# Kernel optimization log

Hardware: AMD Instinct MI355X
Metric: run time of the kernel (lower is better)

The kernel has to match this reference:

```python
import jax, jax.numpy as jnp
import numpy as np

B, S, H, E = 8, 512, 1024, 8
T = B * S            # total tokens
CAP = T // E         # capacity, capacity_factor = 1.0


def _moe(x, wg, ew1, eb1, ew2, eb2):
    # x: [T, H] tokens; top-1 gating with capacity, DeepSpeed-style dispatch/combine
    gates = jax.nn.softmax(x @ wg)                      # [T, E]
    idx = jnp.argmax(gates, axis=-1)                    # [T]
    mask1 = jax.nn.one_hot(idx, E, dtype=x.dtype)       # [T, E]
    locations = jnp.cumsum(mask1, axis=0) - 1.0         # position within expert queue
    mask1 = mask1 * (locations < CAP).astype(x.dtype)   # drop overflow tokens
    gates1 = jnp.sum(gates * mask1, axis=-1)            # [T] combine weight
    locs = jnp.sum(locations * mask1, axis=-1).astype(jnp.int32)  # [T]
    loc_oh = jax.nn.one_hot(locs, CAP, dtype=x.dtype)   # [T, C]
    combine = gates1[:, None, None] * mask1[:, :, None] * loc_oh[:, None, :]  # [T,E,C]
    dispatch = (combine > 0).astype(x.dtype)            # [T, E, C]
    xd = jnp.einsum('sec,sm->ecm', dispatch, x)         # gather tokens per expert
    h = jnp.einsum('ecm,emn->ecn', xd, ew1) + eb1[:, None, :]
    h = jnp.einsum('ecn,enp->ecp', h, ew2) + eb2[:, None, :]
    return jnp.einsum('sec,ecm->sm', combine, h)        # scatter back, weighted


def setup_inputs() -> dict:
    key = jax.random.key(0)
    ks = jax.random.split(key, 16)
    w = lambda k, shape: jax.random.normal(k, shape, jnp.float32) * 0.02
    return {
        'x': jax.random.normal(ks[0], (B, S, H), jnp.float32),
        'y': jax.random.randint(ks[1], (B,), 0, H),
        'w1': w(ks[2], (H, H)), 'b1': jnp.zeros((H,), jnp.float32),
        'w2': w(ks[3], (H, H)), 'b2': jnp.zeros((H,), jnp.float32),
        'w3': w(ks[4], (H, H)), 'b3': jnp.zeros((H,), jnp.float32),
        'wg1': w(ks[5], (H, E)),
        'e1_w1': w(ks[6], (E, H, H)), 'e1_b1': jnp.zeros((E, H), jnp.float32),
        'e1_w2': w(ks[7], (E, H, H)), 'e1_b2': jnp.zeros((E, H), jnp.float32),
        'wg2': w(ks[8], (H, E)),
        'e2_w1': w(ks[9], (E, H, H)), 'e2_b1': jnp.zeros((E, H), jnp.float32),
        'e2_w2': w(ks[10], (E, H, H)), 'e2_b2': jnp.zeros((E, H), jnp.float32),
    }


def reference(x, y, w1, b1, w2, b2, w3, b3, wg1, e1_w1, e1_b1, e1_w2, e1_b2,
              wg2, e2_w1, e2_b1, e2_w2, e2_b2):
    xf = x.reshape(-1, H)                               # [T, H]
    hidden = xf @ w1 + b1
    out = _moe(hidden, wg1, e1_w1, e1_b1, e1_w2, e1_b2)
    out = out @ w2 + b2
    out = _moe(out, wg2, e2_w1, e2_b1, e2_w2, e2_b2)
    out = out @ w3 + b3
    hidden = hidden + out
    sent = hidden.reshape(B, S, H).mean(axis=1)         # [B, H] logits
    logp = jax.nn.log_softmax(sent, axis=-1)
    return -jnp.mean(logp[jnp.arange(B), y])
```

## Files before the change

kernel.cpp:

```cpp
#include <hip/hip_runtime.h>

#define TOK 4096
#define HID 1024
#define NEXP 8
#define CAP 512
#define WSZ 1048576

typedef _Float16 f16;
typedef f16 f16x8 __attribute__((ext_vector_type(8)));
typedef f16 f16x4 __attribute__((ext_vector_type(4)));
typedef f16 f16x2 __attribute__((ext_vector_type(2)));
typedef float f32x4 __attribute__((ext_vector_type(4)));

typedef const __attribute__((address_space(1))) void gvoid;
typedef __attribute__((address_space(3))) void lvoid;

__device__ __forceinline__ void gld16(const void* g, void* l) {
  __builtin_amdgcn_global_load_lds((gvoid*)g, (lvoid*)l, 16, 0, 0);
}

template<int MODE>
__global__ __launch_bounds__(512, 1) void gemm_fused(
    const f16* __restrict__ A, const f16* __restrict__ Bt,
    const float* __restrict__ bias, f16* __restrict__ C,
    const int* __restrict__ rowmap, const float* __restrict__ gmax,
    int rowsPerExpert, long bStride, int biasStride,
    const float* __restrict__ tsrc, f16* __restrict__ tdst, int nGemm)
{
  __shared__ __align__(16) unsigned char smem[65536];
  const int tid = threadIdx.x;

  if ((int)blockIdx.x >= nGemm) {
    float (*t)[65] = (float (*)[65])smem;
    const int tb = blockIdx.x - nGemm;
    const int mat = tb >> 7, t7 = tb & 127;
    const int nb = (t7 & 7) * 128, kb = (t7 >> 3) * 64;
    const float* src = tsrc + (size_t)mat * WSZ;
    f16* d = tdst + (size_t)mat * WSZ;
    const int half = tid >> 8, tl = tid & 255;
    const int rr = tl >> 4, c4 = (tl & 15) * 4;
    float (*th)[65] = t + half * 64;
    float4 v[4];
    #pragma unroll
    for (int p = 0; p < 4; ++p)
      v[p] = *(const float4*)&src[(size_t)(kb + p * 16 + rr) * HID + nb + half * 64 + c4];
    #pragma unroll
    for (int p = 0; p < 4; ++p) {
      th[p * 16 + rr][c4 + 0] = v[p].x;
      th[p * 16 + rr][c4 + 1] = v[p].y;
      th[p * 16 + rr][c4 + 2] = v[p].z;
      th[p * 16 + rr][c4 + 3] = v[p].w;
    }
    __syncthreads();
    #pragma unroll
    for (int it = 0; it < 2; ++it) {
      const int p = it * 256 + tl;
      const int n = p >> 3, kc = p & 7;
      f16x8 o;
      #pragma unroll
      for (int j = 0; j < 8; ++j) o[j] = (f16)th[kc * 8 + j][n];
      *(f16x8*)&d[(size_t)(nb + half * 64 + n) * HID + kb + kc * 8] = o;
    }
    return;
  }

  f16* As0 = (f16*)smem;
  f16* Bs0 = (f16*)(smem + 32768);
  const int w = tid >> 6, l = tid & 63;
  const int wr = w >> 2, wc = w & 3;

  const int orig = blockIdx.x;
  const int sw = (orig & 7) * 32 + (orig >> 3);
  const int bx = sw & 7, by = sw >> 3;
  const int e = (by * 128) / rowsPerExpert;

  const int lr = l >> 3;
  const int chunkSw = ((l & 7) ^ lr) * 8;

  const f16* pst[4];
  if (w < 4) {
    #pragma unroll
    for (int i = 0; i < 4; ++i) {
      int r = by * 128 + w * 32 + i * 8 + lr;
      long tok = r;
      if (MODE == 1) { int t = rowmap[r]; tok = (t < 0) ? (long)TOK : (long)t; }
      pst[i] = A + tok * HID + chunkSw;
    }
  } else {
    #pragma unroll
    for (int i = 0; i < 4; ++i)
      pst[i] = Bt + (size_t)e * bStride
             + (size_t)(bx * 128 + (w - 4) * 32 + i * 8 + lr) * HID + chunkSw;
  }

  f32x4 acc[4][2];
  #pragma unroll
  for (int i = 0; i < 4; ++i)
    #pragma unroll
    for (int j = 0; j < 2; ++j) acc[i][j] = (f32x4){0.f, 0.f, 0.f, 0.f};

  const int g = l >> 4, c = l & 15, sa = c & 7;

  {
    f16* db = (w < 4) ? As0 + (w * 32) * 64 : Bs0 + ((w - 4) * 32) * 64;
    #pragma unroll
    for (int i = 0; i < 4; ++i) gld16(pst[i], db + i * 8 * 64);
  }

  int cur = 0;
  for (int t = 0; t < 15; ++t) {
    {
      const int k0 = (t + 1) * 64;
      f16* db = (w < 4) ? As0 + ((cur ^ 1) * 8192) + (w * 32) * 64
                        : Bs0 + ((cur ^ 1) * 8192) + ((w - 4) * 32) * 64;
      #pragma unroll
      for (int i = 0; i < 4; ++i) gld16(pst[i] + k0, db + i * 8 * 64);
    }
    asm volatile("s_waitcnt vmcnt(4)" ::: "memory");
    asm volatile("s_barrier" ::: "memory");
    __builtin_amdgcn_s_setprio(1);
    #pragma unroll
    for (int h = 0; h < 2; ++h) {
      const int q = ((h * 4 + g) ^ sa) * 8;
      f16x8 af[4], bf[2];
      #pragma unroll
      for (int mi = 0; mi < 4; ++mi)
        af[mi] = *(const f16x8*)&As0[cur * 8192 + (wr * 64 + mi * 16 + c) * 64 + q];
      #pragma unroll
      for (int ni = 0; ni < 2; ++ni)
        bf[ni] = *(const f16x8*)&Bs0[cur * 8192 + (wc * 32 + ni * 16 + c) * 64 + q];
      #pragma unroll
      for (int mi = 0; mi < 4; ++mi)
        #pragma unroll
        for (int ni = 0; ni < 2; ++ni)
          acc[mi][ni] = __builtin_amdgcn_mfma_f32_16x16x32_f16(
              af[mi], bf[ni], acc[mi][ni], 0, 0, 0);
    }
    __builtin_amdgcn_s_setprio(0);
    asm volatile("s_barrier" ::: "memory");
    cur ^= 1;
  }
  asm volatile("s_waitcnt vmcnt(0)" ::: "memory");
  asm volatile("s_barrier" ::: "memory");
  __builtin_amdgcn_s_setprio(1);
  #pragma unroll
  for (int h = 0; h < 2; ++h) {
    const int q = ((h * 4 + g) ^ sa) * 8;
    f16x8 af[4], bf[2];
    #pragma unroll
    for (int mi = 0; mi < 4; ++mi)
      af[mi] = *(const f16x8*)&As0[cur * 8192 + (wr * 64 + mi * 16 + c) * 64 + q];
    #pragma unroll
    for (int ni = 0; ni < 2; ++ni)
      bf[ni] = *(const f16x8*)&Bs0[cur * 8192 + (wc * 32 + ni * 16 + c) * 64 + q];
    #pragma unroll
    for (int mi = 0; mi < 4; ++mi)
      #pragma unroll
      for (int ni = 0; ni < 2; ++ni)
        acc[mi][ni] = __builtin_amdgcn_mfma_f32_16x16x32_f16(
            af[mi], bf[ni], acc[mi][ni], 0, 0, 0);
  }
  __builtin_amdgcn_s_setprio(0);

  int tk[4][4];
  float gv[4][4];
  if (MODE == 2) {
    #pragma unroll
    for (int mi = 0; mi < 4; ++mi)
      #pragma unroll
      for (int rr = 0; rr < 4; ++rr) {
        int r = by * 128 + wr * 64 + mi * 16 + g * 4 + rr;
        int t = rowmap[r];
        tk[mi][rr] = t;
        gv[mi][rr] = (t >= 0) ? gmax[t] : 0.f;
      }
  }
  #pragma unroll
  for (int ni = 0; ni < 2; ++ni) {
    const int col = bx * 128 + wc * 32 + ni * 16 + c;
    const float bv = bias[(size_t)e * biasStride + col];
    #pragma unroll
    for (int mi = 0; mi < 4; ++mi) {
      #pragma unroll
      for (int rr = 0; rr < 4; ++rr) {
        const float v = acc[mi][ni][rr] + bv;
        if (MODE == 2) {
          if (tk[mi][rr] >= 0)
            C[(size_t)tk[mi][rr] * HID + col] = (f16)(v * gv[mi][rr]);
        } else {
          const int row = by * 128 + wr * 64 + mi * 16 + g * 4 + rr;
          C[(size_t)row * HID + col] = (f16)v;
        }
      }
    }
  }
}

__global__ __launch_bounds__(256) void prep2(
    const float* __restrict__ x, f16* __restrict__ X0,
    f16* __restrict__ c1, f16* __restrict__ c2,
    f16* __restrict__ p1, f16* __restrict__ p2,
    const float* __restrict__ w1, const float* __restrict__ w2,
    const float* __restrict__ w3, f16* __restrict__ WT)
{
  __shared__ float t[64][65];
  const int tid = threadIdx.x;
  if ((int)blockIdx.x < 2048) {
    const f16x8 zz = {0, 0, 0, 0, 0, 0, 0, 0};
    #pragma unroll
    for (int it = 0; it < 2; ++it) {
      const size_t i = (size_t)blockIdx.x * 256 + tid + (size_t)it * 524288;
      float4 v = *(const float4*)&x[i * 4];
      f16x4 o = {(f16)v.x, (f16)v.y, (f16)v.z, (f16)v.w};
      *(f16x4*)&X0[i * 4] = o;
      if (i < 524288) { ((f16x8*)c1)[i] = zz; ((f16x8*)c2)[i] = zz; }
      if (i < 128)    { ((f16x8*)p1)[i] = zz; ((f16x8*)p2)[i] = zz; }
    }
    return;
  }
  const int zb = blockIdx.x - 2048;
  const int z = zb >> 8, t7 = zb & 255;
  const float* src = (z == 0) ? w1 : (z == 1) ? w2 : w3;
  f16* d = WT + (size_t)z * WSZ;
  const int kb = (t7 >> 4) * 64, nb = (t7 & 15) * 64;
  const int rr = tid >> 4, c4 = (tid & 15) * 4;
  float4 v[4];
  #pragma unroll
  for (int p = 0; p < 4; ++p)
    v[p] = *(const float4*)&src[(size_t)(kb + p * 16 + rr) * HID + nb + c4];
  #pragma unroll
  for (int p = 0; p < 4; ++p) {
    t[p * 16 + rr][c4 + 0] = v[p].x;
    t[p * 16 + rr][c4 + 1] = v[p].y;
    t[p * 16 + rr][c4 + 2] = v[p].z;
    t[p * 16 + rr][c4 + 3] = v[p].w;
  }
  __syncthreads();
  #pragma unroll
  for (int half = 0; half < 2; ++half) {
    const int p = half * 256 + tid;
    const int n = p >> 3, kc = p & 7;
    f16x8 o;
    #pragma unroll
    for (int j = 0; j < 8; ++j) o[j] = (f16)t[kc * 8 + j][n];
    *(f16x8*)&d[(size_t)(nb + n) * HID + kb + kc * 8] = o;
  }
}

__global__ __launch_bounds__(256) void gate_kernel(
    const f16* __restrict__ act, const float* __restrict__ wg,
    int* __restrict__ idx, float* __restrict__ gmax)
{
  const int tid = threadIdx.x;
  const int tok = blockIdx.x * 8 + (tid >> 5);
  const int sl = tid & 31;
  const f16* row = act + (size_t)tok * HID + sl * 32;
  float xv[32];
  #pragma unroll
  for (int v = 0; v < 4; ++v) {
    f16x8 hv = *(const f16x8*)(row + v * 8);
    #pragma unroll
    for (int j = 0; j < 8; ++j) xv[v * 8 + j] = (float)hv[j];
  }
  float p[NEXP];
  #pragma unroll
  for (int e = 0; e < NEXP; ++e) p[e] = 0.f;
  const float4* w4 = (const float4*)(wg + (size_t)(sl * 32) * NEXP);
  #pragma unroll
  for (int j = 0; j < 32; ++j) {
    float4 lo = w4[2 * j], hi = w4[2 * j + 1];
    p[0] += xv[j] * lo.x; p[1] += xv[j] * lo.y;
    p[2] += xv[j] * lo.z; p[3] += xv[j] * lo.w;
    p[4] += xv[j] * hi.x; p[5] += xv[j] * hi.y;
    p[6] += xv[j] * hi.z; p[7] += xv[j] * hi.w;
  }
  #pragma unroll
  for (int m = 1; m < 32; m <<= 1) {
    #pragma unroll
    for (int e = 0; e < NEXP; ++e) p[e] += __shfl_xor(p[e], m, 64);
  }
  if (sl == 0) {
    float mx = p[0]; int am = 0;
    #pragma unroll
    for (int e = 1; e < NEXP; ++e)
      if (p[e] > mx) { mx = p[e]; am = e; }
    float s = 0.f;
    #pragma unroll
    for (int e = 0; e < NEXP; ++e) s += expf(p[e] - mx);
    idx[tok] = am;
    gmax[tok] = 1.f / s;
  }
}

__global__ __launch_bounds__(512) void scan_kernel(
    const int* __restrict__ idx, int* __restrict__ rowmap)
{
  __shared__ int sidx[TOK];
  const int tid = threadIdx.x;
  for (int i = tid; i < TOK; i += 512) sidx[i] = idx[i];
  for (int i = tid; i < NEXP * CAP; i += 512) rowmap[i] = -1;
  __syncthreads();
  const int wave = tid >> 6, lane = tid & 63;
  int running = 0;
  for (int ch = 0; ch < TOK / 64; ++ch) {
    int t = ch * 64 + lane;
    bool flag = (sidx[t] == wave);
    unsigned long long m = __ballot(flag);
    int pos = running + __popcll(m & ((1ull << lane) - 1ull));
    if (flag && pos < CAP) rowmap[wave * CAP + pos] = t;
    running += __popcll(m);
  }
}

__global__ __launch_bounds__(256) void meanHC_kernel(
    const f16* __restrict__ Hb, const f16* __restrict__ C2b,
    float* __restrict__ pH, float* __restrict__ pC)
{
  const int h2 = blockIdx.x * 256 + threadIdx.x;
  const int b = blockIdx.y, sc = blockIdx.z;
  const f16x2* pa = (const f16x2*)(Hb + ((size_t)b * 512 + sc * 32) * HID) + h2;
  const f16x2* pc = (const f16x2*)(C2b + ((size_t)b * 512 + sc * 32) * HID) + h2;
  float a0 = 0.f, a1 = 0.f, c0 = 0.f, c1 = 0.f;
  #pragma unroll 4
  for (int s = 0; s < 32; ++s) {
    f16x2 va = pa[(size_t)s * 512];
    f16x2 vc = pc[(size_t)s * 512];
    a0 += (float)va[0]; a1 += (float)va[1];
    c0 += (float)vc[0]; c1 += (float)vc[1];
  }
  float* oh = pH + ((size_t)sc * 8 + b) * HID;
  float* oc = pC + ((size_t)sc * 8 + b) * HID;
  oh[h2 * 2] = a0; oh[h2 * 2 + 1] = a1;
  oc[h2 * 2] = c0; oc[h2 * 2 + 1] = c1;
}

__global__ __launch_bounds__(256) void sent_kernel(
    const float* __restrict__ pH, const float* __restrict__ pC,
    const f16* __restrict__ WT2, const float* __restrict__ b3,
    float* __restrict__ sent)
{
  __shared__ float c2m[HID];
  const int tid = threadIdx.x;
  const int b = blockIdx.x >> 2, ch = blockIdx.x & 3;
  for (int kk = tid; kk < HID; kk += 256) {
    float s = 0.f;
    #pragma unroll
    for (int sc = 0; sc < 16; ++sc) s += pC[((size_t)sc * 8 + b) * HID + kk];
    c2m[kk] = s * (1.f / 512.f);
  }
  __syncthreads();
  const int col = ch * 256 + tid;
  float hv = 0.f;
  #pragma unroll
  for (int sc = 0; sc < 16; ++sc) hv += pH[((size_t)sc * 8 + b) * HID + col];
  float acc = hv * (1.f / 512.f) + b3[col];
  const f16* wrow = WT2 + (size_t)col * HID;
  for (int k0 = 0; k0 < HID; k0 += 8) {
    f16x8 wv = *(const f16x8*)(wrow + k0);
    #pragma unroll
    for (int j = 0; j < 8; ++j) acc += c2m[k0 + j] * (float)wv[j];
  }
  sent[b * HID + col] = acc;
}

__global__ __launch_bounds__(1024) void loss_kernel(
    const float* __restrict__ sent, const int* __restrict__ y,
    float* __restrict__ out)
{
  __shared__ float red[17];
  const int tid = threadIdx.x;
  const int wid = tid >> 6, lane = tid & 63;
  float loss = 0.0f;
  for (int b = 0; b < 8; ++b) {
    const float v = sent[b * HID + tid];
    float m = v;
    #pragma unroll
    for (int o = 32; o; o >>= 1) m = fmaxf(m, __shfl_xor(m, o, 64));
    if (lane == 0) red[wid] = m;
    __syncthreads();
    if (tid < 16) {
      float mm = red[tid];
      #pragma unroll
      for (int o = 8; o; o >>= 1) mm = fmaxf(mm, __shfl_xor(mm, o, 16));
      if (tid == 0) red[16] = mm;
    }
    __syncthreads();
    const float M = red[16];
    float s = expf(v - M);
    #pragma unroll
    for (int o = 32; o; o >>= 1) s += __shfl_xor(s, o, 64);
    __syncthreads();
    if (lane == 0) red[wid] = s;
    __syncthreads();
    if (tid < 16) {
      float ss = red[tid];
      #pragma unroll
      for (int o = 8; o; o >>= 1) ss += __shfl_xor(ss, o, 16);
      if (tid == 0) red[16] = M + logf(ss);
    }
    __syncthreads();
    if (tid == 0) loss += -(sent[b * HID + y[b]] - red[16]);
    __syncthreads();
  }
  if (tid == 0) out[0] = loss * (1.0f / 8.0f);
}

extern "C" void kernel_launch(void* const* d_in, const int* in_sizes, int n_in,
                              void* d_out, int out_size, void* d_ws, size_t ws_size,
                              hipStream_t stream)
{
  const float* x    = (const float*)d_in[0];
  const int*   y    = (const int*)d_in[1];
  const float* w1   = (const float*)d_in[2];
  const float* b1   = (const float*)d_in[3];
  const float* w2   = (const float*)d_in[4];
  const float* b2   = (const float*)d_in[5];
  const float* w3   = (const float*)d_in[6];
  const float* b3   = (const float*)d_in[7];
  const float* wg1  = (const float*)d_in[8];
  const float* e1w1 = (const float*)d_in[9];
  const float* e1b1 = (const float*)d_in[10];
  const float* e1w2 = (const float*)d_in[11];
  const float* e1b2 = (const float*)d_in[12];
  const float* wg2  = (const float*)d_in[13];
  const float* e2w1 = (const float*)d_in[14];
  const float* e2b1 = (const float*)d_in[15];
  const float* e2w2 = (const float*)d_in[16];
  const float* e2b2 = (const float*)d_in[17];

  f16* WT = (f16*)d_ws;
  f16* X0 = WT + (size_t)35 * WSZ;
  f16* H  = X0 + (size_t)TOK * HID;
  f16* EA = H + (size_t)(TOK + 1) * HID;
  f16* C1 = EA + (size_t)TOK * HID;
  f16* M1 = C1 + (size_t)TOK * HID;
  f16* C2 = M1 + (size_t)(TOK + 1) * HID;
  float* gmax  = (float*)(C2 + (size_t)TOK * HID);
  int* idx     = (int*)(gmax + TOK);
  int* rowmap  = idx + TOK;
  float* sent  = (float*)(rowmap + TOK);
  float* pH    = sent + 8 * HID;
  float* pC    = pH + 16 * 8 * HID;

  f16* WTe1a = WT + (size_t)3 * WSZ;
  f16* WTe1b = WT + (size_t)11 * WSZ;
  f16* WTe2a = WT + (size_t)19 * WSZ;
  f16* WTe2b = WT + (size_t)27 * WSZ;

  const int FUSED = 256 + 8 * 128;

  prep2<<<2816, 256, 0, stream>>>(x, X0, C1, C2,
                                  H + (size_t)TOK * HID, M1 + (size_t)TOK * HID,
                                  w1, w2, w3, WT);

  gemm_fused<0><<<FUSED, 512, 0, stream>>>(X0, WT, b1, H, nullptr, nullptr,
                                           TOK, 0, 0, e1w1, WTe1a, 256);

  gate_kernel<<<512, 256, 0, stream>>>(H, wg1, idx, gmax);
  scan_kernel<<<1, 512, 0, stream>>>(idx, rowmap);
  gemm_fused<1><<<FUSED, 512, 0, stream>>>(H, WTe1a, e1b1, EA, rowmap, nullptr,
                                           CAP, WSZ, HID, e1w2, WTe1b, 256);
  gemm_fused<2><<<FUSED, 512, 0, stream>>>(EA, WTe1b, e1b2, C1, rowmap, gmax,
                                           CAP, WSZ, HID, e2w1, WTe2a, 256);

  gemm_fused<0><<<FUSED, 512, 0, stream>>>(C1, WT + (size_t)1 * WSZ, b2, M1,
                                           nullptr, nullptr, TOK, 0, 0,
                                           e2w2, WTe2b, 256);

  gate_kernel<<<512, 256, 0, stream>>>(M1, wg2, idx, gmax);
  scan_kernel<<<1, 512, 0, stream>>>(idx, rowmap);
  gemm_fused<1><<<256, 512, 0, stream>>>(M1, WTe2a, e2b1, EA, rowmap, nullptr,
                                         CAP, WSZ, HID, w1, WT, 256);
  gemm_fused<2><<<256, 512, 0, stream>>>(EA, WTe2b, e2b2, C2, rowmap, gmax,
                                         CAP, WSZ, HID, w1, WT, 256);

  meanHC_kernel<<<dim3(2, 8, 16), 256, 0, stream>>>(H, C2, pH, pC);
  sent_kernel<<<32, 256, 0, stream>>>(pH, pC, WT + (size_t)2 * WSZ, b3, sent);
  loss_kernel<<<1, 1024, 0, stream>>>(sent, y, (float*)d_out);
}
```

Before: 218.4 us.

## Fold gate projection into preceding weight and fuse gating/scan into GEMM launch

```diff
diff --git a/kernel.cpp b/kernel.cpp
--- a/kernel.cpp
+++ b/kernel.cpp
@@ -25,10 +25,80 @@
     const float* __restrict__ bias, f16* __restrict__ C,
     const int* __restrict__ rowmap, const float* __restrict__ gmax,
     int rowsPerExpert, long bStride, int biasStride,
-    const float* __restrict__ tsrc, f16* __restrict__ tdst, int nGemm)
+    const float* __restrict__ tsrc, f16* __restrict__ tdst,
+    const f16* __restrict__ gX, const float* __restrict__ G,
+    const float* __restrict__ Gb, int* __restrict__ gidx,
+    float* __restrict__ ggmax, int* __restrict__ grm,
+    int* __restrict__ counter, int nGemm, int nTrans, int nGate)
 {
   __shared__ __align__(16) unsigned char smem[65536];
   const int tid = threadIdx.x;
+
+  if ((int)blockIdx.x >= nGemm + nTrans) {
+    const int gb = blockIdx.x - nGemm - nTrans;
+    const int tok = gb * 16 + (tid >> 5);
+    const int sl = tid & 31;
+    const f16* row = gX + (size_t)tok * HID + sl * 32;
+    float xv[32];
+    #pragma unroll
+    for (int v = 0; v < 4; ++v) {
+      f16x8 hv = *(const f16x8*)(row + v * 8);
+      #pragma unroll
+      for (int j = 0; j < 8; ++j) xv[v * 8 + j] = (float)hv[j];
+    }
+    float p[NEXP];
+    #pragma unroll
+    for (int e = 0; e < NEXP; ++e) p[e] = 0.f;
+    const float4* g4 = (const float4*)(G + (size_t)(sl * 32) * NEXP);
+    #pragma unroll
+    for (int j = 0; j < 32; ++j) {
+      float4 lo = g4[2 * j], hi = g4[2 * j + 1];
+      p[0] += xv[j] * lo.x; p[1] += xv[j] * lo.y;
+      p[2] += xv[j] * lo.z; p[3] += xv[j] * lo.w;
+      p[4] += xv[j] * hi.x; p[5] += xv[j] * hi.y;
+      p[6] += xv[j] * hi.z; p[7] += xv[j] * hi.w;
+    }
+    #pragma unroll
+    for (int m = 1; m < 32; m <<= 1) {
+      #pragma unroll
+      for (int e = 0; e < NEXP; ++e) p[e] += __shfl_xor(p[e], m, 64);
+    }
+    if (sl == 0) {
+      #pragma unroll
+      for (int e = 0; e < NEXP; ++e) p[e] += Gb[e];
+      float mx = p[0]; int am = 0;
+      #pragma unroll
+      for (int e = 1; e < NEXP; ++e)
+        if (p[e] > mx) { mx = p[e]; am = e; }
+      float s = 0.f;
+      #pragma unroll
+      for (int e = 0; e < NEXP; ++e) s += expf(p[e] - mx);
+      gidx[tok] = am;
+      ggmax[tok] = 1.f / s;
+    }
+    __threadfence();
+    __syncthreads();
+    int* sflag = (int*)(smem + 32768);
+    if (tid == 0) sflag[0] = (atomicAdd(counter, 1) == nGate - 1) ? 1 : 0;
+    __syncthreads();
+    if (!sflag[0]) return;
+    __threadfence();
+    int* sidx = (int*)smem;
+    for (int i = tid; i < TOK; i += 512) sidx[i] = gidx[i];
+    for (int i = tid; i < NEXP * CAP; i += 512) grm[i] = -1;
+    __syncthreads();
+    const int wave = tid >> 6, lane = tid & 63;
+    int running = 0;
+    for (int ch = 0; ch < TOK / 64; ++ch) {
+      int t = ch * 64 + lane;
+      bool flag = (sidx[t] == wave);
+      unsigned long long m = __ballot(flag);
+      int pos = running + __popcll(m & ((1ull << lane) - 1ull));
+      if (flag && pos < CAP) grm[wave * CAP + pos] = t;
+      running += __popcll(m);
+    }
+    return;
+  }
 
   if ((int)blockIdx.x >= nGemm) {
     float (*t)[65] = (float (*)[65])smem;
@@ -201,11 +271,17 @@
     f16* __restrict__ c1, f16* __restrict__ c2,
     f16* __restrict__ p1, f16* __restrict__ p2,
     const float* __restrict__ w1, const float* __restrict__ w2,
-    const float* __restrict__ w3, f16* __restrict__ WT)
+    const float* __restrict__ w3, f16* __restrict__ WT,
+    const float* __restrict__ wg1, const float* __restrict__ wg2,
+    const float* __restrict__ b1, const float* __restrict__ b2,
+    float* __restrict__ G1, float* __restrict__ G2,
+    float* __restrict__ Gb1, float* __restrict__ Gb2,
+    int* __restrict__ counters)
 {
-  __shared__ float t[64][65];
+  __shared__ float sh[8192];
   const int tid = threadIdx.x;
   if ((int)blockIdx.x < 2048) {
+    if (blockIdx.x == 0 && tid < 2) counters[tid] = 0;
     const f16x8 zz = {0, 0, 0, 0, 0, 0, 0, 0};
     #pragma unroll
     for (int it = 0; it < 2; ++it) {
@@ -218,97 +294,59 @@
     }
     return;
   }
-  const int zb = blockIdx.x - 2048;
-  const int z = zb >> 8, t7 = zb & 255;
-  const float* src = (z == 0) ? w1 : (z == 1) ? w2 : w3;
-  f16* d = WT + (size_t)z * WSZ;
-  const int kb = (t7 >> 4) * 64, nb = (t7 & 15) * 64;
-  const int rr = tid >> 4, c4 = (tid & 15) * 4;
-  float4 v[4];
-  #pragma unroll
-  for (int p = 0; p < 4; ++p)
-    v[p] = *(const float4*)&src[(size_t)(kb + p * 16 + rr) * HID + nb + c4];
-  #pragma unroll
-  for (int p = 0; p < 4; ++p) {
-    t[p * 16 + rr][c4 + 0] = v[p].x;
-    t[p * 16 + rr][c4 + 1] = v[p].y;
-    t[p * 16 + rr][c4 + 2] = v[p].z;
-    t[p * 16 + rr][c4 + 3] = v[p].w;
-  }
+  if ((int)blockIdx.x < 2816) {
+    const int zb = blockIdx.x - 2048;
+    const int z = zb >> 8, t7 = zb & 255;
+    const float* src = (z == 0) ? w1 : (z == 1) ? w2 : w3;
+    f16* d = WT + (size_t)z * WSZ;
+    const int kb = (t7 >> 4) * 64, nb = (t7 & 15) * 64;
+    const int rr = tid >> 4, c4 = (tid & 15) * 4;
+    float4 v[4];
+    #pragma unroll
+    for (int p = 0; p < 4; ++p)
+      v[p] = *(const float4*)&src[(size_t)(kb + p * 16 + rr) * HID + nb + c4];
+    #pragma unroll
+    for (int p = 0; p < 4; ++p) {
+      sh[(p * 16 + rr) * 65 + c4 + 0] = v[p].x;
+      sh[(p * 16 + rr) * 65 + c4 + 1] = v[p].y;
+      sh[(p * 16 + rr) * 65 + c4 + 2] = v[p].z;
+      sh[(p * 16 + rr) * 65 + c4 + 3] = v[p].w;
+    }
+    __syncthreads();
+    #pragma unroll
+    for (int half = 0; half < 2; ++half) {
+      const int p = half * 256 + tid;
+      const int n = p >> 3, kc = p & 7;
+      f16x8 o;
+      #pragma unroll
+      for (int j = 0; j < 8; ++j) o[j] = (f16)sh[(kc * 8 + j) * 65 + n];
+      *(f16x8*)&d[(size_t)(nb + n) * HID + kb + kc * 8] = o;
+    }
+    return;
+  }
+  const int gz = blockIdx.x - 2816;
+  const int which = gz >> 5;
+  const int kb = (gz & 31) * 32;
+  const float* w  = which ? w2 : w1;
+  const float* wg = which ? wg2 : wg1;
+  const float* b  = which ? b2 : b1;
+  float* Gout  = which ? G2 : G1;
+  float* GbOut = which ? Gb2 : Gb1;
+  for (int i = tid; i < 8192; i += 256) sh[i] = wg[i];
   __syncthreads();
-  #pragma unroll
-  for (int half = 0; half < 2; ++half) {
-    const int p = half * 256 + tid;
-    const int n = p >> 3, kc = p & 7;
-    f16x8 o;
-    #pragma unroll
-    for (int j = 0; j < 8; ++j) o[j] = (f16)t[kc * 8 + j][n];
-    *(f16x8*)&d[(size_t)(nb + n) * HID + kb + kc * 8] = o;
-  }
-}
-
-__global__ __launch_bounds__(256) void gate_kernel(
-    const f16* __restrict__ act, const float* __restrict__ wg,
-    int* __restrict__ idx, float* __restrict__ gmax)
-{
-  const int tid = threadIdx.x;
-  const int tok = blockIdx.x * 8 + (tid >> 5);
-  const int sl = tid & 31;
-  const f16* row = act + (size_t)tok * HID + sl * 32;
-  float xv[32];
-  #pragma unroll
-  for (int v = 0; v < 4; ++v) {
-    f16x8 hv = *(const f16x8*)(row + v * 8);
-    #pragma unroll
-    for (int j = 0; j < 8; ++j) xv[v * 8 + j] = (float)hv[j];
-  }
-  float p[NEXP];
-  #pragma unroll
-  for (int e = 0; e < NEXP; ++e) p[e] = 0.f;
-  const float4* w4 = (const float4*)(wg + (size_t)(sl * 32) * NEXP);
-  #pragma unroll
-  for (int j = 0; j < 32; ++j) {
-    float4 lo = w4[2 * j], hi = w4[2 * j + 1];
-    p[0] += xv[j] * lo.x; p[1] += xv[j] * lo.y;
-    p[2] += xv[j] * lo.z; p[3] += xv[j] * lo.w;
-    p[4] += xv[j] * hi.x; p[5] += xv[j] * hi.y;
-    p[6] += xv[j] * hi.z; p[7] += xv[j] * hi.w;
-  }
-  #pragma unroll
-  for (int m = 1; m < 32; m <<= 1) {
-    #pragma unroll
-    for (int e = 0; e < NEXP; ++e) p[e] += __shfl_xor(p[e], m, 64);
-  }
-  if (sl == 0) {
-    float mx = p[0]; int am = 0;
-    #pragma unroll
-    for (int e = 1; e < NEXP; ++e)
-      if (p[e] > mx) { mx = p[e]; am = e; }
+  const int k = kb + (tid >> 3), ee = tid & 7;
+  const float4* wrow = (const float4*)(w + (size_t)k * HID);
+  float acc = 0.f;
+  for (int m4 = 0; m4 < 256; ++m4) {
+    float4 wv = wrow[m4];
+    acc += wv.x * sh[(m4 * 4 + 0) * 8 + ee] + wv.y * sh[(m4 * 4 + 1) * 8 + ee]
+         + wv.z * sh[(m4 * 4 + 2) * 8 + ee] + wv.w * sh[(m4 * 4 + 3) * 8 + ee];
+  }
+  Gout[k * 8 + ee] = acc;
+  if (kb == 0 && tid < 8) {
     float s = 0.f;
-    #pragma unroll
-    for (int e = 0; e < NEXP; ++e) s += expf(p[e] - mx);
-    idx[tok] = am;
-    gmax[tok] = 1.f / s;
-  }
-}
-
-__global__ __launch_bounds__(512) void scan_kernel(
-    const int* __restrict__ idx, int* __restrict__ rowmap)
-{
-  __shared__ int sidx[TOK];
-  const int tid = threadIdx.x;
-  for (int i = tid; i < TOK; i += 512) sidx[i] = idx[i];
-  for (int i = tid; i < NEXP * CAP; i += 512) rowmap[i] = -1;
-  __syncthreads();
-  const int wave = tid >> 6, lane = tid & 63;
-  int running = 0;
-  for (int ch = 0; ch < TOK / 64; ++ch) {
-    int t = ch * 64 + lane;
-    bool flag = (sidx[t] == wave);
-    unsigned long long m = __ballot(flag);
-    int pos = running + __popcll(m & ((1ull << lane) - 1ull));
-    if (flag && pos < CAP) rowmap[wave * CAP + pos] = t;
-    running += __popcll(m);
+    for (int m = 0; m < HID; ++m) s += b[m] * sh[m * 8 + tid];
+    GbOut[tid] = s;
   }
 }
 
@@ -435,10 +473,18 @@
   f16* C1 = EA + (size_t)TOK * HID;
   f16* M1 = C1 + (size_t)TOK * HID;
   f16* C2 = M1 + (size_t)(TOK + 1) * HID;
-  float* gmax  = (float*)(C2 + (size_t)TOK * HID);
-  int* idx     = (int*)(gmax + TOK);
-  int* rowmap  = idx + TOK;
-  float* sent  = (float*)(rowmap + TOK);
+  float* gmax1 = (float*)(C2 + (size_t)TOK * HID);
+  float* gmax2 = gmax1 + TOK;
+  int* idx1    = (int*)(gmax2 + TOK);
+  int* idx2    = idx1 + TOK;
+  int* rm1     = idx2 + TOK;
+  int* rm2     = rm1 + NEXP * CAP;
+  int* counters = rm2 + NEXP * CAP;
+  float* G1    = (float*)(counters + 16);
+  float* G2    = G1 + HID * NEXP;
+  float* Gb1   = G2 + HID * NEXP;
+  float* Gb2   = Gb1 + 8;
+  float* sent  = Gb2 + 8;
   float* pH    = sent + 8 * HID;
   float* pC    = pH + 16 * 8 * HID;
 
@@ -447,32 +493,40 @@
   f16* WTe2a = WT + (size_t)19 * WSZ;
   f16* WTe2b = WT + (size_t)27 * WSZ;
 
-  const int FUSED = 256 + 8 * 128;
-
-  prep2<<<2816, 256, 0, stream>>>(x, X0, C1, C2,
+  prep2<<<2880, 256, 0, stream>>>(x, X0, C1, C2,
                                   H + (size_t)TOK * HID, M1 + (size_t)TOK * HID,
-                                  w1, w2, w3, WT);
-
-  gemm_fused<0><<<FUSED, 512, 0, stream>>>(X0, WT, b1, H, nullptr, nullptr,
-                                           TOK, 0, 0, e1w1, WTe1a, 256);
-
-  gate_kernel<<<512, 256, 0, stream>>>(H, wg1, idx, gmax);
-  scan_kernel<<<1, 512, 0, stream>>>(idx, rowmap);
-  gemm_fused<1><<<FUSED, 512, 0, stream>>>(H, WTe1a, e1b1, EA, rowmap, nullptr,
-                                           CAP, WSZ, HID, e1w2, WTe1b, 256);
-  gemm_fused<2><<<FUSED, 512, 0, stream>>>(EA, WTe1b, e1b2, C1, rowmap, gmax,
-                                           CAP, WSZ, HID, e2w1, WTe2a, 256);
-
-  gemm_fused<0><<<FUSED, 512, 0, stream>>>(C1, WT + (size_t)1 * WSZ, b2, M1,
-                                           nullptr, nullptr, TOK, 0, 0,
-                                           e2w2, WTe2b, 256);
-
-  gate_kernel<<<512, 256, 0, stream>>>(M1, wg2, idx, gmax);
-  scan_kernel<<<1, 512, 0, stream>>>(idx, rowmap);
-  gemm_fused<1><<<256, 512, 0, stream>>>(M1, WTe2a, e2b1, EA, rowmap, nullptr,
-                                         CAP, WSZ, HID, w1, WT, 256);
-  gemm_fused<2><<<256, 512, 0, stream>>>(EA, WTe2b, e2b2, C2, rowmap, gmax,
-                                         CAP, WSZ, HID, w1, WT, 256);
+                                  w1, w2, w3, WT, wg1, wg2, b1, b2,
+                                  G1, G2, Gb1, Gb2, counters);
+
+  gemm_fused<0><<<256 + 1024 + 256, 512, 0, stream>>>(
+      X0, WT, b1, H, nullptr, nullptr, TOK, 0, 0,
+      e1w1, WTe1a, X0, G1, Gb1, idx1, gmax1, rm1, counters + 0,
+      256, 1024, 256);
+
+  gemm_fused<1><<<256 + 1024, 512, 0, stream>>>(
+      H, WTe1a, e1b1, EA, rm1, nullptr, CAP, WSZ, HID,
+      e1w2, WTe1b, nullptr, nullptr, nullptr, nullptr, nullptr, nullptr, nullptr,
+      256, 1024, 0);
+
+  gemm_fused<2><<<256 + 1024, 512, 0, stream>>>(
+      EA, WTe1b, e1b2, C1, rm1, gmax1, CAP, WSZ, HID,
+      e2w1, WTe2a, nullptr, nullptr, nullptr, nullptr, nullptr, nullptr, nullptr,
+      256, 1024, 0);
+
+  gemm_fused<0><<<256 + 1024 + 256, 512, 0, stream>>>(
+      C1, WT + (size_t)1 * WSZ, b2, M1, nullptr, nullptr, TOK, 0, 0,
+      e2w2, WTe2b, C1, G2, Gb2, idx2, gmax2, rm2, counters + 1,
+      256, 1024, 256);
+
+  gemm_fused<1><<<256, 512, 0, stream>>>(
+      M1, WTe2a, e2b1, EA, rm2, nullptr, CAP, WSZ, HID,
+      nullptr, nullptr, nullptr, nullptr, nullptr, nullptr, nullptr, nullptr, nullptr,
+      256, 0, 0);
+
+  gemm_fused<2><<<256, 512, 0, stream>>>(
+      EA, WTe2b, e2b2, C2, rm2, gmax2, CAP, WSZ, HID,
+      nullptr, nullptr, nullptr, nullptr, nullptr, nullptr, nullptr, nullptr, nullptr,
+      256, 0, 0);
 
   meanHC_kernel<<<dim3(2, 8, 16), 256, 0, stream>>>(H, C2, pH, pC);
   sent_kernel<<<32, 256, 0, stream>>>(pH, pC, WT + (size_t)2 * WSZ, b3, sent);
```

New measurement: 325.4 us. 49.0% more time.

## Shrink GEMM tiles to 64x128 with 256-thread blocks for multi-block occupancy

Applied to the files above, without the earlier changes.

```diff
diff --git a/kernel.cpp b/kernel.cpp
--- a/kernel.cpp
+++ b/kernel.cpp
@@ -20,78 +20,70 @@
 }
 
 template<int MODE>
-__global__ __launch_bounds__(512, 1) void gemm_fused(
+__global__ __launch_bounds__(256, 3) void gemm_fused(
     const f16* __restrict__ A, const f16* __restrict__ Bt,
     const float* __restrict__ bias, f16* __restrict__ C,
     const int* __restrict__ rowmap, const float* __restrict__ gmax,
     int rowsPerExpert, long bStride, int biasStride,
     const float* __restrict__ tsrc, f16* __restrict__ tdst, int nGemm)
 {
-  __shared__ __align__(16) unsigned char smem[65536];
+  __shared__ __align__(16) unsigned char smem[49152];
   const int tid = threadIdx.x;
 
   if ((int)blockIdx.x >= nGemm) {
     float (*t)[65] = (float (*)[65])smem;
     const int tb = blockIdx.x - nGemm;
-    const int mat = tb >> 7, t7 = tb & 127;
-    const int nb = (t7 & 7) * 128, kb = (t7 >> 3) * 64;
+    const int mat = tb >> 8, t8 = tb & 255;
+    const int kb = (t8 >> 4) * 64, nb = (t8 & 15) * 64;
     const float* src = tsrc + (size_t)mat * WSZ;
     f16* d = tdst + (size_t)mat * WSZ;
-    const int half = tid >> 8, tl = tid & 255;
-    const int rr = tl >> 4, c4 = (tl & 15) * 4;
-    float (*th)[65] = t + half * 64;
+    const int rr = tid >> 4, c4 = (tid & 15) * 4;
     float4 v[4];
     #pragma unroll
     for (int p = 0; p < 4; ++p)
-      v[p] = *(const float4*)&src[(size_t)(kb + p * 16 + rr) * HID + nb + half * 64 + c4];
+      v[p] = *(const float4*)&src[(size_t)(kb + p * 16 + rr) * HID + nb + c4];
     #pragma unroll
     for (int p = 0; p < 4; ++p) {
-      th[p * 16 + rr][c4 + 0] = v[p].x;
-      th[p * 16 + rr][c4 + 1] = v[p].y;
-      th[p * 16 + rr][c4 + 2] = v[p].z;
-      th[p * 16 + rr][c4 + 3] = v[p].w;
-    }
-    __syncthreads();
-    #pragma unroll
-    for (int it = 0; it < 2; ++it) {
-      const int p = it * 256 + tl;
+      t[p * 16 + rr][c4 + 0] = v[p].x;
+      t[p * 16 + rr][c4 + 1] = v[p].y;
+      t[p * 16 + rr][c4 + 2] = v[p].z;
+      t[p * 16 + rr][c4 + 3] = v[p].w;
+    }
+    __syncthreads();
+    #pragma unroll
+    for (int half = 0; half < 2; ++half) {
+      const int p = half * 256 + tid;
       const int n = p >> 3, kc = p & 7;
       f16x8 o;
       #pragma unroll
-      for (int j = 0; j < 8; ++j) o[j] = (f16)th[kc * 8 + j][n];
-      *(f16x8*)&d[(size_t)(nb + half * 64 + n) * HID + kb + kc * 8] = o;
+      for (int j = 0; j < 8; ++j) o[j] = (f16)t[kc * 8 + j][n];
+      *(f16x8*)&d[(size_t)(nb + n) * HID + kb + kc * 8] = o;
     }
     return;
   }
 
   f16* As0 = (f16*)smem;
-  f16* Bs0 = (f16*)(smem + 32768);
+  f16* Bs0 = (f16*)(smem + 16384);
   const int w = tid >> 6, l = tid & 63;
-  const int wr = w >> 2, wc = w & 3;
 
   const int orig = blockIdx.x;
-  const int sw = (orig & 7) * 32 + (orig >> 3);
+  const int sw = (orig & 7) * 64 + (orig >> 3);
   const int bx = sw & 7, by = sw >> 3;
-  const int e = (by * 128) / rowsPerExpert;
+  const int e = (by * 64) / rowsPerExpert;
 
   const int lr = l >> 3;
   const int chunkSw = ((l & 7) ^ lr) * 8;
 
-  const f16* pst[4];
-  if (w < 4) {
-    #pragma unroll
-    for (int i = 0; i < 4; ++i) {
-      int r = by * 128 + w * 32 + i * 8 + lr;
-      long tok = r;
-      if (MODE == 1) { int t = rowmap[r]; tok = (t < 0) ? (long)TOK : (long)t; }
-      pst[i] = A + tok * HID + chunkSw;
-    }
-  } else {
-    #pragma unroll
-    for (int i = 0; i < 4; ++i)
-      pst[i] = Bt + (size_t)e * bStride
-             + (size_t)(bx * 128 + (w - 4) * 32 + i * 8 + lr) * HID + chunkSw;
-  }
+  const f16* pa[2];
+  #pragma unroll
+  for (int i = 0; i < 2; ++i) {
+    int r = by * 64 + w * 16 + i * 8 + lr;
+    long tok = r;
+    if (MODE == 1) { int t = rowmap[r]; tok = (t < 0) ? (long)TOK : (long)t; }
+    pa[i] = A + tok * HID + chunkSw;
+  }
+  const f16* pb = Bt + (size_t)e * bStride
+                + (size_t)(bx * 128 + w * 32 + lr) * HID + chunkSw;
 
   f32x4 acc[4][2];
   #pragma unroll
@@ -102,21 +94,26 @@
   const int g = l >> 4, c = l & 15, sa = c & 7;
 
   {
-    f16* db = (w < 4) ? As0 + (w * 32) * 64 : Bs0 + ((w - 4) * 32) * 64;
-    #pragma unroll
-    for (int i = 0; i < 4; ++i) gld16(pst[i], db + i * 8 * 64);
+    f16* ab = As0 + (w * 16) * 64;
+    f16* bb = Bs0 + (w * 32) * 64;
+    #pragma unroll
+    for (int i = 0; i < 2; ++i) gld16(pa[i], ab + i * 8 * 64);
+    #pragma unroll
+    for (int i = 0; i < 4; ++i) gld16(pb + (size_t)(i * 8) * HID, bb + i * 8 * 64);
   }
 
   int cur = 0;
   for (int t = 0; t < 15; ++t) {
     {
       const int k0 = (t + 1) * 64;
-      f16* db = (w < 4) ? As0 + ((cur ^ 1) * 8192) + (w * 32) * 64
-                        : Bs0 + ((cur ^ 1) * 8192) + ((w - 4) * 32) * 64;
-      #pragma unroll
-      for (int i = 0; i < 4; ++i) gld16(pst[i] + k0, db + i * 8 * 64);
-    }
-    asm volatile("s_waitcnt vmcnt(4)" ::: "memory");
+      f16* ab = As0 + (cur ^ 1) * 4096 + (w * 16) * 64;
+      f16* bb = Bs0 + (cur ^ 1) * 8192 + (w * 32) * 64;
+      #pragma unroll
+      for (int i = 0; i < 2; ++i) gld16(pa[i] + k0, ab + i * 8 * 64);
+      #pragma unroll
+      for (int i = 0; i < 4; ++i) gld16(pb + (size_t)(i * 8) * HID + k0, bb + i * 8 * 64);
+    }
+    asm volatile("s_waitcnt vmcnt(6)" ::: "memory");
     asm volatile("s_barrier" ::: "memory");
     __builtin_amdgcn_s_setprio(1);
     #pragma unroll
@@ -125,10 +122,10 @@
       f16x8 af[4], bf[2];
       #pragma unroll
       for (int mi = 0; mi < 4; ++mi)
-        af[mi] = *(const f16x8*)&As0[cur * 8192 + (wr * 64 + mi * 16 + c) * 64 + q];
+        af[mi] = *(const f16x8*)&As0[cur * 4096 + (mi * 16 + c) * 64 + q];
       #pragma unroll
       for (int ni = 0; ni < 2; ++ni)
-        bf[ni] = *(const f16x8*)&Bs0[cur * 8192 + (wc * 32 + ni * 16 + c) * 64 + q];
+        bf[ni] = *(const f16x8*)&Bs0[cur * 8192 + (w * 32 + ni * 16 + c) * 64 + q];
       #pragma unroll
       for (int mi = 0; mi < 4; ++mi)
         #pragma unroll
@@ -149,10 +146,10 @@
     f16x8 af[4], bf[2];
     #pragma unroll
     for (int mi = 0; mi < 4; ++mi)
-      af[mi] = *(const f16x8*)&As0[cur * 8192 + (wr * 64 + mi * 16 + c) * 64 + q];
+      af[mi] = *(const f16x8*)&As0[cur * 4096 + (mi * 16 + c) * 64 + q];
     #pragma unroll
     for (int ni = 0; ni < 2; ++ni)
-      bf[ni] = *(const f16x8*)&Bs0[cur * 8192 + (wc * 32 + ni * 16 + c) * 64 + q];
+      bf[ni] = *(const f16x8*)&Bs0[cur * 8192 + (w * 32 + ni * 16 + c) * 64 + q];
     #pragma unroll
     for (int mi = 0; mi < 4; ++mi)
       #pragma unroll
@@ -169,7 +166,7 @@
     for (int mi = 0; mi < 4; ++mi)
       #pragma unroll
       for (int rr = 0; rr < 4; ++rr) {
-        int r = by * 128 + wr * 64 + mi * 16 + g * 4 + rr;
+        int r = by * 64 + mi * 16 + g * 4 + rr;
         int t = rowmap[r];
         tk[mi][rr] = t;
         gv[mi][rr] = (t >= 0) ? gmax[t] : 0.f;
@@ -177,7 +174,7 @@
   }
   #pragma unroll
   for (int ni = 0; ni < 2; ++ni) {
-    const int col = bx * 128 + wc * 32 + ni * 16 + c;
+    const int col = bx * 128 + w * 32 + ni * 16 + c;
     const float bv = bias[(size_t)e * biasStride + col];
     #pragma unroll
     for (int mi = 0; mi < 4; ++mi) {
@@ -188,7 +185,7 @@
           if (tk[mi][rr] >= 0)
             C[(size_t)tk[mi][rr] * HID + col] = (f16)(v * gv[mi][rr]);
         } else {
-          const int row = by * 128 + wr * 64 + mi * 16 + g * 4 + rr;
+          const int row = by * 64 + mi * 16 + g * 4 + rr;
           C[(size_t)row * HID + col] = (f16)v;
         }
       }
@@ -219,10 +216,10 @@
     return;
   }
   const int zb = blockIdx.x - 2048;
-  const int z = zb >> 8, t7 = zb & 255;
+  const int z = zb >> 8, t8 = zb & 255;
   const float* src = (z == 0) ? w1 : (z == 1) ? w2 : w3;
   f16* d = WT + (size_t)z * WSZ;
-  const int kb = (t7 >> 4) * 64, nb = (t7 & 15) * 64;
+  const int kb = (t8 >> 4) * 64, nb = (t8 & 15) * 64;
   const int rr = tid >> 4, c4 = (tid & 15) * 4;
   float4 v[4];
   #pragma unroll
@@ -438,7 +435,7 @@
   float* gmax  = (float*)(C2 + (size_t)TOK * HID);
   int* idx     = (int*)(gmax + TOK);
   int* rowmap  = idx + TOK;
-  float* sent  = (float*)(rowmap + TOK);
+  float* sent  = (float*)(rowmap + NEXP * CAP);
   float* pH    = sent + 8 * HID;
   float* pC    = pH + 16 * 8 * HID;
 
@@ -447,32 +444,32 @@
   f16* WTe2a = WT + (size_t)19 * WSZ;
   f16* WTe2b = WT + (size_t)27 * WSZ;
 
-  const int FUSED = 256 + 8 * 128;
+  const int FUSED = 512 + 8 * 256;
 
   prep2<<<2816, 256, 0, stream>>>(x, X0, C1, C2,
                                   H + (size_t)TOK * HID, M1 + (size_t)TOK * HID,
                                   w1, w2, w3, WT);
 
-  gemm_fused<0><<<FUSED, 512, 0, stream>>>(X0, WT, b1, H, nullptr, nullptr,
-                                           TOK, 0, 0, e1w1, WTe1a, 256);
+  gemm_fused<0><<<FUSED, 256, 0, stream>>>(X0, WT, b1, H, nullptr, nullptr,
+                                           TOK, 0, 0, e1w1, WTe1a, 512);
 
   gate_kernel<<<512, 256, 0, stream>>>(H, wg1, idx, gmax);
   scan_kernel<<<1, 512, 0, stream>>>(idx, rowmap);
-  gemm_fused<1><<<FUSED, 512, 0, stream>>>(H, WTe1a, e1b1, EA, rowmap, nullptr,
-                                           CAP, WSZ, HID, e1w2, WTe1b, 256);
-  gemm_fused<2><<<FUSED, 512, 0, stream>>>(EA, WTe1b, e1b2, C1, rowmap, gmax,
-                                           CAP, WSZ, HID, e2w1, WTe2a, 256);
-
-  gemm_fused<0><<<FUSED, 512, 0, stream>>>(C1, WT + (size_t)1 * WSZ, b2, M1,
+  gemm_fused<1><<<FUSED, 256, 0, stream>>>(H, WTe1a, e1b1, EA, rowmap, nullptr,
+                                           CAP, WSZ, HID, e1w2, WTe1b, 512);
+  gemm_fused<2><<<FUSED, 256, 0, stream>>>(EA, WTe1b, e1b2, C1, rowmap, gmax,
+                                           CAP, WSZ, HID, e2w1, WTe2a, 512);
+
+  gemm_fused<0><<<FUSED, 256, 0, stream>>>(C1, WT + (size_t)1 * WSZ, b2, M1,
                                            nullptr, nullptr, TOK, 0, 0,
-                                           e2w2, WTe2b, 256);
+                                           e2w2, WTe2b, 512);
 
   gate_kernel<<<512, 256, 0, stream>>>(M1, wg2, idx, gmax);
   scan_kernel<<<1, 512, 0, stream>>>(idx, rowmap);
-  gemm_fused<1><<<256, 512, 0, stream>>>(M1, WTe2a, e2b1, EA, rowmap, nullptr,
-                                         CAP, WSZ, HID, w1, WT, 256);
-  gemm_fused<2><<<256, 512, 0, stream>>>(EA, WTe2b, e2b2, C2, rowmap, gmax,
-                                         CAP, WSZ, HID, w1, WT, 256);
+  gemm_fused<1><<<512, 256, 0, stream>>>(M1, WTe2a, e2b1, EA, rowmap, nullptr,
+                                         CAP, WSZ, HID, w1, WT, 512);
+  gemm_fused<2><<<512, 256, 0, stream>>>(EA, WTe2b, e2b2, C2, rowmap, gmax,
+                                         CAP, WSZ, HID, w1, WT, 512);
 
   meanHC_kernel<<<dim3(2, 8, 16), 256, 0, stream>>>(H, C2, pH, pC);
   sent_kernel<<<32, 256, 0, stream>>>(pH, pC, WT + (size_t)2 * WSZ, b3, sent);
```

Measured after the change: 226.0 us. 1.03x slower.

## Pipeline weight transpose with async LDS loads over 256-row slabs

Applied to the files above, without the earlier changes.

```diff
diff --git a/kernel.cpp b/kernel.cpp
--- a/kernel.cpp
+++ b/kernel.cpp
@@ -17,6 +17,44 @@
 
 __device__ __forceinline__ void gld16(const void* g, void* l) {
   __builtin_amdgcn_global_load_lds((gvoid*)g, (lvoid*)l, 16, 0, 0);
+}
+
+__device__ __forceinline__ void wtrans(const float* __restrict__ src,
+                                       f16* __restrict__ dst,
+                                       int nb, int kb0, float* lds, int tid)
+{
+  const int n = tid >> 3, seg = tid & 7;
+  #define WSTAGE(ks, buf)                                                    \
+    {                                                                        \
+      _Pragma("unroll")                                                      \
+      for (int i = 0; i < 2; ++i) {                                          \
+        int p = i * 512 + tid;                                               \
+        int r = p >> 4, c = p & 15;                                          \
+        int cg = c ^ ((r >> 2) & 15);                                        \
+        gld16(src + (size_t)(kb0 + (ks) * 64 + r) * HID + nb + cg * 4,       \
+              lds + (buf) * 4096 + p * 4);                                   \
+      }                                                                      \
+    }
+  WSTAGE(0, 0);
+  #pragma unroll
+  for (int s = 0; s < 4; ++s) {
+    if (s == 0)      { WSTAGE(1, 1); asm volatile("s_waitcnt vmcnt(2)" ::: "memory"); }
+    else if (s == 1) { WSTAGE(2, 0); asm volatile("s_waitcnt vmcnt(3)" ::: "memory"); }
+    else if (s == 2) { WSTAGE(3, 1); asm volatile("s_waitcnt vmcnt(3)" ::: "memory"); }
+    else             {               asm volatile("s_waitcnt vmcnt(1)" ::: "memory"); }
+    asm volatile("s_barrier" ::: "memory");
+    const float* B = lds + (s & 1) * 4096;
+    f16x8 o;
+    #pragma unroll
+    for (int j = 0; j < 8; ++j) {
+      int r = seg * 8 + j;
+      int cl = (n >> 2) ^ ((r >> 2) & 15);
+      o[j] = (f16)B[r * 64 + cl * 4 + (n & 3)];
+    }
+    *(f16x8*)&dst[(size_t)(nb + n) * HID + kb0 + s * 64 + seg * 8] = o;
+    asm volatile("s_barrier" ::: "memory");
+  }
+  #undef WSTAGE
 }
 
 template<int MODE>
@@ -31,36 +69,10 @@
   const int tid = threadIdx.x;
 
   if ((int)blockIdx.x >= nGemm) {
-    float (*t)[65] = (float (*)[65])smem;
     const int tb = blockIdx.x - nGemm;
-    const int mat = tb >> 7, t7 = tb & 127;
-    const int nb = (t7 & 7) * 128, kb = (t7 >> 3) * 64;
-    const float* src = tsrc + (size_t)mat * WSZ;
-    f16* d = tdst + (size_t)mat * WSZ;
-    const int half = tid >> 8, tl = tid & 255;
-    const int rr = tl >> 4, c4 = (tl & 15) * 4;
-    float (*th)[65] = t + half * 64;
-    float4 v[4];
-    #pragma unroll
-    for (int p = 0; p < 4; ++p)
-      v[p] = *(const float4*)&src[(size_t)(kb + p * 16 + rr) * HID + nb + half * 64 + c4];
-    #pragma unroll
-    for (int p = 0; p < 4; ++p) {
-      th[p * 16 + rr][c4 + 0] = v[p].x;
-      th[p * 16 + rr][c4 + 1] = v[p].y;
-      th[p * 16 + rr][c4 + 2] = v[p].z;
-      th[p * 16 + rr][c4 + 3] = v[p].w;
-    }
-    __syncthreads();
-    #pragma unroll
-    for (int it = 0; it < 2; ++it) {
-      const int p = it * 256 + tl;
-      const int n = p >> 3, kc = p & 7;
-      f16x8 o;
-      #pragma unroll
-      for (int j = 0; j < 8; ++j) o[j] = (f16)th[kc * 8 + j][n];
-      *(f16x8*)&d[(size_t)(nb + half * 64 + n) * HID + kb + kc * 8] = o;
-    }
+    const int mat = tb >> 6, slab = tb & 63;
+    wtrans(tsrc + (size_t)mat * WSZ, tdst + (size_t)mat * WSZ,
+           (slab & 15) * 64, (slab >> 4) * 256, (float*)smem, tid);
     return;
   }
 
@@ -196,55 +208,35 @@
   }
 }
 
-__global__ __launch_bounds__(256) void prep2(
+__global__ __launch_bounds__(512) void prep2(
     const float* __restrict__ x, f16* __restrict__ X0,
     f16* __restrict__ c1, f16* __restrict__ c2,
     f16* __restrict__ p1, f16* __restrict__ p2,
     const float* __restrict__ w1, const float* __restrict__ w2,
     const float* __restrict__ w3, f16* __restrict__ WT)
 {
-  __shared__ float t[64][65];
-  const int tid = threadIdx.x;
-  if ((int)blockIdx.x < 2048) {
+  __shared__ __align__(16) float lds[2 * 4096];
+  const int tid = threadIdx.x;
+  if ((int)blockIdx.x < 1024) {
     const f16x8 zz = {0, 0, 0, 0, 0, 0, 0, 0};
+    const size_t i = (size_t)blockIdx.x * 512 + tid;
     #pragma unroll
     for (int it = 0; it < 2; ++it) {
-      const size_t i = (size_t)blockIdx.x * 256 + tid + (size_t)it * 524288;
-      float4 v = *(const float4*)&x[i * 4];
+      const size_t idx = i + (size_t)it * 524288;
+      float4 v = *(const float4*)&x[idx * 4];
       f16x4 o = {(f16)v.x, (f16)v.y, (f16)v.z, (f16)v.w};
-      *(f16x4*)&X0[i * 4] = o;
-      if (i < 524288) { ((f16x8*)c1)[i] = zz; ((f16x8*)c2)[i] = zz; }
-      if (i < 128)    { ((f16x8*)p1)[i] = zz; ((f16x8*)p2)[i] = zz; }
-    }
+      *(f16x4*)&X0[idx * 4] = o;
+    }
+    ((f16x8*)c1)[i] = zz;
+    ((f16x8*)c2)[i] = zz;
+    if (i < 128) { ((f16x8*)p1)[i] = zz; ((f16x8*)p2)[i] = zz; }
     return;
   }
-  const int zb = blockIdx.x - 2048;
-  const int z = zb >> 8, t7 = zb & 255;
+  const int tb = blockIdx.x - 1024;
+  const int z = tb >> 6, slab = tb & 63;
   const float* src = (z == 0) ? w1 : (z == 1) ? w2 : w3;
-  f16* d = WT + (size_t)z * WSZ;
-  const int kb = (t7 >> 4) * 64, nb = (t7 & 15) * 64;
-  const int rr = tid >> 4, c4 = (tid & 15) * 4;
-  float4 v[4];
-  #pragma unroll
-  for (int p = 0; p < 4; ++p)
-    v[p] = *(const float4*)&src[(size_t)(kb + p * 16 + rr) * HID + nb + c4];
-  #pragma unroll
-  for (int p = 0; p < 4; ++p) {
-    t[p * 16 + rr][c4 + 0] = v[p].x;
-    t[p * 16 + rr][c4 + 1] = v[p].y;
-    t[p * 16 + rr][c4 + 2] = v[p].z;
-    t[p * 16 + rr][c4 + 3] = v[p].w;
-  }
-  __syncthreads();
-  #pragma unroll
-  for (int half = 0; half < 2; ++half) {
-    const int p = half * 256 + tid;
-    const int n = p >> 3, kc = p & 7;
-    f16x8 o;
-    #pragma unroll
-    for (int j = 0; j < 8; ++j) o[j] = (f16)t[kc * 8 + j][n];
-    *(f16x8*)&d[(size_t)(nb + n) * HID + kb + kc * 8] = o;
-  }
+  wtrans(src, WT + (size_t)z * WSZ, (slab & 15) * 64, (slab >> 4) * 256,
+         lds, tid);
 }
 
 __global__ __launch_bounds__(256) void gate_kernel(
@@ -438,7 +430,7 @@
   float* gmax  = (float*)(C2 + (size_t)TOK * HID);
   int* idx     = (int*)(gmax + TOK);
   int* rowmap  = idx + TOK;
-  float* sent  = (float*)(rowmap + TOK);
+  float* sent  = (float*)(rowmap + NEXP * CAP);
   float* pH    = sent + 8 * HID;
   float* pC    = pH + 16 * 8 * HID;
 
@@ -447,9 +439,9 @@
   f16* WTe2a = WT + (size_t)19 * WSZ;
   f16* WTe2b = WT + (size_t)27 * WSZ;
 
-  const int FUSED = 256 + 8 * 128;
-
-  prep2<<<2816, 256, 0, stream>>>(x, X0, C1, C2,
+  const int FUSED = 256 + 512;
+
+  prep2<<<1216, 512, 0, stream>>>(x, X0, C1, C2,
                                   H + (size_t)TOK * HID, M1 + (size_t)TOK * HID,
                                   w1, w2, w3, WT);
 
```

Result: no change. 215.4 us (-1.4%).
